# Kernel tuning notes

Measured on AMD Instinct MI355X. Metric: run time of the kernel, lower is better.

## Reference

```python
import jax, jax.numpy as jnp
import numpy as np
import math

CEN_W = 1.0
ANG_W = 1.0


def _radius(ndim):
    # Iterative version of the recursive Radius() from the source.
    if ndim < 1:
        raise ValueError('ndim >= 1 required')
    if ndim == 1:
        return 0.0
    r = 0.5
    for _ in range(3, ndim + 1):
        r = 0.5 / math.sqrt(1.0 - r * r)
    return r


def _costheta(ndim):
    return 2.0 * _radius(ndim - 1) ** 2 - 1.0


def setup_inputs() -> dict:
    key = jax.random.key(0)
    k1, k2, k3 = jax.random.split(key, 3)
    B, C, D = 65536, 1000, 512
    y = jax.random.randint(k1, (B,), 0, C, dtype=jnp.int64 if jax.config.jax_enable_x64 else jnp.int32)
    feat = jax.random.normal(k2, (B, D), dtype=jnp.float32)
    centers = jax.random.normal(k3, (C, D), dtype=jnp.float32)
    return {"y": y, "feat": feat, "centers": centers}


def reference(y, feat, centers):
    C = centers.shape[0]
    B = feat.shape[0]
    ct = jnp.float32(_costheta(C))  # static Python constant from num_classes

    # ---- center loss: gather assigned centers, squared diff sum ----
    centers_pred = centers[y]                      # [B, D] gather
    diff = feat - centers_pred
    loss_cen = 0.5 * jnp.sum(diff * diff) / B

    # ---- angular loss: vectorized Gram matrix over classes ----
    # In torch, centers[j].data and dist are detached -> stop_gradient here.
    centers_sg = jax.lax.stop_gradient(centers)
    dist = jnp.linalg.norm(centers_sg, axis=1)     # [C], detached
    gram = centers @ centers_sg.T                  # [C, C]; grad flows via rows only
    sim = gram / (dist[:, None] * dist[None, :])
    offdiag = 1.0 - jnp.eye(C, dtype=sim.dtype)
    loss_ang = jnp.sum(offdiag * (sim - ct) ** 2) / (0.5 * C * (C - 1))

    return loss_cen * CEN_W + loss_ang * ANG_W
```

## Files before the change

kernel.cpp:

```cpp
#include <hip/hip_runtime.h>
#include <math.h>

typedef __attribute__((ext_vector_type(8))) short bf16x8;
typedef __attribute__((ext_vector_type(16))) float f32x16;
typedef __attribute__((ext_vector_type(4))) float vf4;
typedef __attribute__((ext_vector_type(4))) unsigned int u32x4;

__device__ __forceinline__ float wave_reduce(float v) {
#pragma unroll
    for (int off = 32; off > 0; off >>= 1) v += __shfl_down(v, off, 64);
    return v;
}

__device__ __forceinline__ unsigned int pk_trunc(float f0, float f1) {
    unsigned u0 = __float_as_uint(f0), u1 = __float_as_uint(f1);
    return (u1 & 0xFFFF0000u) | (u0 >> 16);
}

__global__ __launch_bounds__(256) void fused_kernel(const int* __restrict__ y,
                                                    const vf4* __restrict__ feat4,
                                                    const vf4* __restrict__ cent4,
                                                    float* __restrict__ partials,
                                                    int n4, int d4, float cen_scale,
                                                    int C, int ntile32, int ntri,
                                                    int steps16, float ct, float ang_scale) {
    const int bid = blockIdx.x;
    const int lane = threadIdx.x & 63;
    const int wid = threadIdx.x >> 6;
    __shared__ float sm[4];

    float partial = 0.f;

    const int t = bid * 4 + wid;
    if (t < ntri) {
        const int N = ntile32;
        const float ff = (float)((2 * N + 1) * (2 * N + 1) - 8 * t);
        int ti = (int)(((float)(2 * N + 1) - sqrtf(ff)) * 0.5f);
        int base = ti * N - (ti * (ti - 1)) / 2;
        if (t < base) {
            --ti; base = ti * N - (ti * (ti - 1)) / 2;
        } else {
            const int nxt = (ti + 1) * N - ((ti + 1) * ti) / 2;
            if (t >= nxt) { ++ti; base = nxt; }
        }
        const int tj = ti + (t - base);

        const int m = lane & 31;
        const int half = lane >> 5;
        const int ra = ti * 32 + m;
        const int rb = tj * 32 + m;
        const bool va = ra < C;
        const bool vb = rb < C;
        const vf4* aptr = cent4 + (size_t)ra * d4 + half * 2;
        const vf4* bptr = cent4 + (size_t)rb * d4 + half * 2;
        f32x16 acc;
#pragma unroll
        for (int k = 0; k < 16; ++k) acc[k] = 0.f;
        float sa = 0.f, sb = 0.f;
#pragma unroll 4
        for (int st = 0; st < steps16; ++st) {
            vf4 a0 = {0.f, 0.f, 0.f, 0.f}, a1 = a0, b0 = a0, b1 = a0;
            if (va) { a0 = aptr[st * 4]; a1 = aptr[st * 4 + 1]; }
            if (vb) { b0 = bptr[st * 4]; b1 = bptr[st * 4 + 1]; }
            sa += a0.x * a0.x + a0.y * a0.y + a0.z * a0.z + a0.w * a0.w
                + a1.x * a1.x + a1.y * a1.y + a1.z * a1.z + a1.w * a1.w;
            sb += b0.x * b0.x + b0.y * b0.y + b0.z * b0.z + b0.w * b0.w
                + b1.x * b1.x + b1.y * b1.y + b1.z * b1.z + b1.w * b1.w;
            u32x4 ap, bp;
            ap.x = pk_trunc(a0.x, a0.y); ap.y = pk_trunc(a0.z, a0.w);
            ap.z = pk_trunc(a1.x, a1.y); ap.w = pk_trunc(a1.z, a1.w);
            bp.x = pk_trunc(b0.x, b0.y); bp.y = pk_trunc(b0.z, b0.w);
            bp.z = pk_trunc(b1.x, b1.y); bp.w = pk_trunc(b1.z, b1.w);
            bf16x8 af = __builtin_bit_cast(bf16x8, ap);
            bf16x8 bf = __builtin_bit_cast(bf16x8, bp);
            acc = __builtin_amdgcn_mfma_f32_32x32x16_bf16(af, bf, acc, 0, 0, 0);
        }
        sa += __shfl_xor(sa, 32, 64);
        sb += __shfl_xor(sb, 32, 64);
        const int gj = tj * 32 + m;
        const float dj = sb;
        float local = 0.f;
#pragma unroll
        for (int reg = 0; reg < 16; ++reg) {
            const int r = (reg & 3) + 8 * (reg >> 2) + 4 * half;
            const int gi = ti * 32 + r;
            const float di = __shfl(sa, r, 64);
            if (gi < C && gj < C && gi != gj) {
                float sim = acc[reg] * rsqrtf(di * dj);
                float dlt = sim - ct;
                local += dlt * dlt;
            }
        }
        const float w = (ti == tj) ? 1.f : 2.f;
        partial = local * (ang_scale * w);
    }

    {
        const int stride = gridDim.x * 256;
        float cs = 0.f;
        int i = bid * 256 + threadIdx.x;
        const bool fast = ((stride % d4) == 0) && ((d4 & 63) == 0) && (n4 == 4 * stride);
        if (fast) {
            int row = i / d4;
            const int col = i - row * d4;
            const int rstep = stride / d4;
            const vf4 f0 = __builtin_nontemporal_load(feat4 + i);
            const vf4 f1 = __builtin_nontemporal_load(feat4 + i + stride);
            const vf4 f2 = __builtin_nontemporal_load(feat4 + i + 2 * stride);
            const vf4 f3 = __builtin_nontemporal_load(feat4 + i + 3 * stride);
            const int r0 = __builtin_amdgcn_readfirstlane(row);
            const int cls0 = y[r0];
            const int cls1 = y[r0 + rstep];
            const int cls2 = y[r0 + 2 * rstep];
            const int cls3 = y[r0 + 3 * rstep];
            const vf4 g0 = cent4[(size_t)cls0 * d4 + col];
            const vf4 g1 = cent4[(size_t)cls1 * d4 + col];
            const vf4 g2 = cent4[(size_t)cls2 * d4 + col];
            const vf4 g3 = cent4[(size_t)cls3 * d4 + col];
            float dx, dy, dz, dw;
            dx = f0.x - g0.x; dy = f0.y - g0.y; dz = f0.z - g0.z; dw = f0.w - g0.w;
            cs += dx * dx + dy * dy + dz * dz + dw * dw;
            dx = f1.x - g1.x; dy = f1.y - g1.y; dz = f1.z - g1.z; dw = f1.w - g1.w;
            cs += dx * dx + dy * dy + dz * dz + dw * dw;
            dx = f2.x - g2.x; dy = f2.y - g2.y; dz = f2.z - g2.z; dw = f2.w - g2.w;
            cs += dx * dx + dy * dy + dz * dz + dw * dw;
            dx = f3.x - g3.x; dy = f3.y - g3.y; dz = f3.z - g3.z; dw = f3.w - g3.w;
            cs += dx * dx + dy * dy + dz * dz + dw * dw;
        } else {
            for (; i < n4; i += stride) {
                int row = i / d4;
                int col = i - row * d4;
                const int cls = y[row];
                vf4 f = __builtin_nontemporal_load(feat4 + i);
                vf4 c = cent4[(size_t)cls * d4 + col];
                float dx = f.x - c.x, dy = f.y - c.y, dz = f.z - c.z, dw = f.w - c.w;
                cs += dx * dx + dy * dy + dz * dz + dw * dw;
            }
        }
        partial += cs * cen_scale;
    }

    float r = wave_reduce(partial);
    if (lane == 0) sm[wid] = r;
    __syncthreads();
    if (threadIdx.x == 0) {
        partials[bid] = sm[0] + sm[1] + sm[2] + sm[3];
    }
}

__global__ __launch_bounds__(256) void reduce_kernel(const float* __restrict__ partials,
                                                     float* __restrict__ out, int nb) {
    __shared__ float sm[4];
    const int lane = threadIdx.x & 63;
    const int wid = threadIdx.x >> 6;
    float s = 0.f;
    for (int i = threadIdx.x; i < nb; i += 256) s += partials[i];
    s = wave_reduce(s);
    if (lane == 0) sm[wid] = s;
    __syncthreads();
    if (threadIdx.x == 0) out[0] = sm[0] + sm[1] + sm[2] + sm[3];
}

extern "C" void kernel_launch(void* const* d_in, const int* in_sizes, int n_in,
                              void* d_out, int out_size, void* d_ws, size_t ws_size,
                              hipStream_t stream) {
    const int* y = (const int*)d_in[0];
    const float* feat = (const float*)d_in[1];
    const float* centers = (const float*)d_in[2];

    const int B = in_sizes[0];
    const int D = in_sizes[1] / B;
    const int C = in_sizes[2] / D;
    const int d4 = D / 4;
    const int ntile32 = (C + 31) / 32;
    const int ntri = ntile32 * (ntile32 + 1) / 2;

    const int nd = C - 1;
    double r = 0.0;
    if (nd >= 2) {
        r = 0.5;
        for (int i = 3; i <= nd; ++i) r = 0.5 / sqrt(1.0 - r * r);
    }
    const float ct = (float)(2.0 * r * r - 1.0);

    const float cen_scale = (float)(0.5 / (double)B);
    const float ang_scale = (float)(1.0 / (0.5 * (double)C * (double)(C - 1)));

    float* partials = (float*)d_ws;
    const int nb = 8192;

    fused_kernel<<<nb, 256, 0, stream>>>(
        y, (const vf4*)feat, (const vf4*)centers, partials,
        B * d4, d4, cen_scale, C, ntile32, ntri, D / 16, ct, ang_scale);

    reduce_kernel<<<1, 256, 0, stream>>>(partials, (float*)d_out, nb);
}
```

Baseline: 208.3 us.

## Split fused kernel into separate angular and center-loss kernels

```diff
diff --git a/kernel.cpp b/kernel.cpp
--- a/kernel.cpp
+++ b/kernel.cpp
@@ -17,13 +17,71 @@
     return (u1 & 0xFFFF0000u) | (u0 >> 16);
 }
 
-__global__ __launch_bounds__(256) void fused_kernel(const int* __restrict__ y,
-                                                    const vf4* __restrict__ feat4,
-                                                    const vf4* __restrict__ cent4,
-                                                    float* __restrict__ partials,
-                                                    int n4, int d4, float cen_scale,
-                                                    int C, int ntile32, int ntri,
-                                                    int steps16, float ct, float ang_scale) {
+
+__global__ __launch_bounds__(256, 8) void center_kernel(const int* __restrict__ y,
+                                                        const vf4* __restrict__ feat4,
+                                                        const vf4* __restrict__ cent4,
+                                                        float* __restrict__ partials,
+                                                        int n4, int d4, float cen_scale) {
+    const int bid = blockIdx.x;
+    const int lane = threadIdx.x & 63;
+    const int wid = threadIdx.x >> 6;
+    __shared__ float sm[4];
+
+    const int stride = gridDim.x * 256;
+    float cs = 0.f;
+    int i = bid * 256 + threadIdx.x;
+    const bool fast = ((stride % d4) == 0) && ((d4 & 63) == 0) && (n4 == 4 * stride);
+    if (fast) {
+        int row = i / d4;
+        const int col = i - row * d4;
+        const int rstep = stride / d4;
+        const vf4 f0 = __builtin_nontemporal_load(feat4 + i);
+        const vf4 f1 = __builtin_nontemporal_load(feat4 + i + stride);
+        const vf4 f2 = __builtin_nontemporal_load(feat4 + i + 2 * stride);
+        const vf4 f3 = __builtin_nontemporal_load(feat4 + i + 3 * stride);
+        const int r0 = __builtin_amdgcn_readfirstlane(row);
+        const int cls0 = y[r0];
+        const int cls1 = y[r0 + rstep];
+        const int cls2 = y[r0 + 2 * rstep];
+        const int cls3 = y[r0 + 3 * rstep];
+        const vf4 g0 = cent4[(size_t)cls0 * d4 + col];
+        const vf4 g1 = cent4[(size_t)cls1 * d4 + col];
+        const vf4 g2 = cent4[(size_t)cls2 * d4 + col];
+        const vf4 g3 = cent4[(size_t)cls3 * d4 + col];
+        float dx, dy, dz, dw;
+        dx = f0.x - g0.x; dy = f0.y - g0.y; dz = f0.z - g0.z; dw = f0.w - g0.w;
+        cs += dx * dx + dy * dy + dz * dz + dw * dw;
+        dx = f1.x - g1.x; dy = f1.y - g1.y; dz = f1.z - g1.z; dw = f1.w - g1.w;
+        cs += dx * dx + dy * dy + dz * dz + dw * dw;
+        dx = f2.x - g2.x; dy = f2.y - g2.y; dz = f2.z - g2.z; dw = f2.w - g2.w;
+        cs += dx * dx + dy * dy + dz * dz + dw * dw;
+        dx = f3.x - g3.x; dy = f3.y - g3.y; dz = f3.z - g3.z; dw = f3.w - g3.w;
+        cs += dx * dx + dy * dy + dz * dz + dw * dw;
+    } else {
+        for (; i < n4; i += stride) {
+            int row = i / d4;
+            int col = i - row * d4;
+            const int cls = y[row];
+            vf4 f = __builtin_nontemporal_load(feat4 + i);
+            vf4 c = cent4[(size_t)cls * d4 + col];
+            float dx = f.x - c.x, dy = f.y - c.y, dz = f.z - c.z, dw = f.w - c.w;
+            cs += dx * dx + dy * dy + dz * dz + dw * dw;
+        }
+    }
+
+    float r = wave_reduce(cs * cen_scale);
+    if (lane == 0) sm[wid] = r;
+    __syncthreads();
+    if (threadIdx.x == 0) {
+        partials[bid] = sm[0] + sm[1] + sm[2] + sm[3];
+    }
+}
+
+__global__ __launch_bounds__(256) void ang_kernel(const vf4* __restrict__ cent4,
+                                                  float* __restrict__ partials_ang,
+                                                  int d4, int C, int ntile32, int ntri,
+                                                  int steps16, float ct, float ang_scale) {
     const int bid = blockIdx.x;
     const int lane = threadIdx.x & 63;
     const int wid = threadIdx.x >> 6;
@@ -95,66 +153,21 @@
         partial = local * (ang_scale * w);
     }
 
-    {
-        const int stride = gridDim.x * 256;
-        float cs = 0.f;
-        int i = bid * 256 + threadIdx.x;
-        const bool fast = ((stride % d4) == 0) && ((d4 & 63) == 0) && (n4 == 4 * stride);
-        if (fast) {
-            int row = i / d4;
-            const int col = i - row * d4;
-            const int rstep = stride / d4;
-            const vf4 f0 = __builtin_nontemporal_load(feat4 + i);
-            const vf4 f1 = __builtin_nontemporal_load(feat4 + i + stride);
-            const vf4 f2 = __builtin_nontemporal_load(feat4 + i + 2 * stride);
-            const vf4 f3 = __builtin_nontemporal_load(feat4 + i + 3 * stride);
-            const int r0 = __builtin_amdgcn_readfirstlane(row);
-            const int cls0 = y[r0];
-            const int cls1 = y[r0 + rstep];
-            const int cls2 = y[r0 + 2 * rstep];
-            const int cls3 = y[r0 + 3 * rstep];
-            const vf4 g0 = cent4[(size_t)cls0 * d4 + col];
-            const vf4 g1 = cent4[(size_t)cls1 * d4 + col];
-            const vf4 g2 = cent4[(size_t)cls2 * d4 + col];
-            const vf4 g3 = cent4[(size_t)cls3 * d4 + col];
-            float dx, dy, dz, dw;
-            dx = f0.x - g0.x; dy = f0.y - g0.y; dz = f0.z - g0.z; dw = f0.w - g0.w;
-            cs += dx * dx + dy * dy + dz * dz + dw * dw;
-            dx = f1.x - g1.x; dy = f1.y - g1.y; dz = f1.z - g1.z; dw = f1.w - g1.w;
-            cs += dx * dx + dy * dy + dz * dz + dw * dw;
-            dx = f2.x - g2.x; dy = f2.y - g2.y; dz = f2.z - g2.z; dw = f2.w - g2.w;
-            cs += dx * dx + dy * dy + dz * dz + dw * dw;
-            dx = f3.x - g3.x; dy = f3.y - g3.y; dz = f3.z - g3.z; dw = f3.w - g3.w;
-            cs += dx * dx + dy * dy + dz * dz + dw * dw;
-        } else {
-            for (; i < n4; i += stride) {
-                int row = i / d4;
-                int col = i - row * d4;
-                const int cls = y[row];
-                vf4 f = __builtin_nontemporal_load(feat4 + i);
-                vf4 c = cent4[(size_t)cls * d4 + col];
-                float dx = f.x - c.x, dy = f.y - c.y, dz = f.z - c.z, dw = f.w - c.w;
-                cs += dx * dx + dy * dy + dz * dz + dw * dw;
-            }
-        }
-        partial += cs * cen_scale;
-    }
-
     float r = wave_reduce(partial);
     if (lane == 0) sm[wid] = r;
     __syncthreads();
     if (threadIdx.x == 0) {
-        partials[bid] = sm[0] + sm[1] + sm[2] + sm[3];
+        partials_ang[bid] = sm[0] + sm[1] + sm[2] + sm[3];
     }
 }
 
 __global__ __launch_bounds__(256) void reduce_kernel(const float* __restrict__ partials,
-                                                     float* __restrict__ out, int nb) {
+                                                     float* __restrict__ out, int ntot) {
     __shared__ float sm[4];
     const int lane = threadIdx.x & 63;
     const int wid = threadIdx.x >> 6;
     float s = 0.f;
-    for (int i = threadIdx.x; i < nb; i += 256) s += partials[i];
+    for (int i = threadIdx.x; i < ntot; i += 256) s += partials[i];
     s = wave_reduce(s);
     if (lane == 0) sm[wid] = s;
     __syncthreads();
@@ -186,12 +199,15 @@
     const float cen_scale = (float)(0.5 / (double)B);
     const float ang_scale = (float)(1.0 / (0.5 * (double)C * (double)(C - 1)));
 
+    const int nb_cen = 8192;
+    const int nb_ang = (ntri + 3) / 4;
     float* partials = (float*)d_ws;
-    const int nb = 8192;
-
-    fused_kernel<<<nb, 256, 0, stream>>>(
-        y, (const vf4*)feat, (const vf4*)centers, partials,
-        B * d4, d4, cen_scale, C, ntile32, ntri, D / 16, ct, ang_scale);
-
-    reduce_kernel<<<1, 256, 0, stream>>>(partials, (float*)d_out, nb);
-}
+
+    ang_kernel<<<nb_ang, 256, 0, stream>>>(
+        (const vf4*)centers, partials + nb_cen, d4, C, ntile32, ntri, D / 16, ct, ang_scale);
+
+    center_kernel<<<nb_cen, 256, 0, stream>>>(
+        y, (const vf4*)feat, (const vf4*)centers, partials, B * d4, d4, cen_scale);
+
+    reduce_kernel<<<1, 256, 0, stream>>>(partials, (float*)d_out, nb_cen + nb_ang);
+}
```

Result: slower. 218.1 us (+4.7%).
